# Optimization experiments

Hardware: AMD Instinct MI355X
Metric: run time of the kernel (lower is better)

The kernel has to match this reference:

```python
import jax, jax.numpy as jnp
import numpy as np

B, N, C = 8, 1025, 768
NUM_HEADS = 12
HEAD_DIM = C // NUM_HEADS  # 64, also depthwise-conv channel count
HW = (32, 32)              # N = 1 + 32*32 (cls token)
SCALE = HEAD_DIM ** -0.5
VALUE_MASK_FILL = -10000.0
LN_EPS = 1e-5


def setup_inputs() -> dict:
    key = jax.random.key(0)
    ks = jax.random.split(key, 12)
    s = 0.02
    inp = {
        "x": jax.random.normal(ks[0], (B, N, C), jnp.float32),
        "mask": jax.random.bernoulli(ks[1], 0.9, (B, N)),
        "Wq": jax.random.normal(ks[2], (C, C), jnp.float32) * s,
        "Wk": jax.random.normal(ks[3], (C, C), jnp.float32) * s,
        "Wv": jax.random.normal(ks[4], (C, C), jnp.float32) * s,
        "pool_q_w": jax.random.normal(ks[5], (HEAD_DIM, 1, 3, 3), jnp.float32) * s,
        "pool_k_w": jax.random.normal(ks[6], (HEAD_DIM, 1, 3, 3), jnp.float32) * s,
        "pool_v_w": jax.random.normal(ks[7], (HEAD_DIM, 1, 3, 3), jnp.float32) * s,
        "gq": jnp.ones((HEAD_DIM,), jnp.float32),
        "bq": jnp.zeros((HEAD_DIM,), jnp.float32),
        "gk": jnp.ones((HEAD_DIM,), jnp.float32),
        "bk": jnp.zeros((HEAD_DIM,), jnp.float32),
        "gv": jnp.ones((HEAD_DIM,), jnp.float32),
        "bv": jnp.zeros((HEAD_DIM,), jnp.float32),
        "Wp": jax.random.normal(ks[8], (C, C), jnp.float32) * s,
        "bp": jnp.zeros((C,), jnp.float32),
    }
    return inp


def _layernorm(t, g, b):
    m = jnp.mean(t, axis=-1, keepdims=True)
    v = jnp.var(t, axis=-1, keepdims=True)
    return (t - m) * jax.lax.rsqrt(v + LN_EPS) * g + b


def _depthwise(t, w):
    # t: [BH, D, H, W], w: [D, 1, 3, 3] depthwise, stride 1, SAME padding
    return jax.lax.conv_general_dilated(
        t, w, window_strides=(1, 1), padding="SAME",
        dimension_numbers=("NCHW", "OIHW", "NCHW"),
        feature_group_count=t.shape[1])


def _attn_pool(t, w, g, b):
    # t: [B, H, N, D] with leading cls token; pool spatial tokens, norm after
    Bb, Hh, Nn, D = t.shape
    cls_tok, spat = t[:, :, :1], t[:, :, 1:]
    Hs, Ws = HW
    spat = spat.reshape(Bb * Hh, Hs, Ws, D).transpose(0, 3, 1, 2)
    spat = _depthwise(spat, w)
    spat = spat.reshape(Bb, Hh, D, Hs * Ws).transpose(0, 1, 3, 2)
    t = jnp.concatenate([cls_tok, spat], axis=2)
    return _layernorm(t, g, b)


def reference(x, mask, Wq, Wk, Wv, pool_q_w, pool_k_w, pool_v_w,
              gq, bq, gk, bk, gv, bv, Wp, bp):
    Bb, Nn, Cc = x.shape
    # QKV projections (no bias), split heads -> [B, H, N, D]
    q = (x @ Wq.T).reshape(Bb, Nn, NUM_HEADS, HEAD_DIM).transpose(0, 2, 1, 3)
    k = (x @ Wk.T).reshape(Bb, Nn, NUM_HEADS, HEAD_DIM).transpose(0, 2, 1, 3)
    v = (x @ Wv.T).reshape(Bb, Nn, NUM_HEADS, HEAD_DIM).transpose(0, 2, 1, 3)
    q = _attn_pool(q, pool_q_w, gq, bq)
    k = _attn_pool(k, pool_k_w, gk, bk)
    v = _attn_pool(v, pool_v_w, gv, bv)
    attn = jnp.einsum("bhqd,bhkd->bhqk", q, k) * SCALE
    # mask: [B, N] bool; broadcast as (B,1,N,1), False -> value_mask_fill
    attn = jnp.where(mask[:, None, :, None], attn, VALUE_MASK_FILL)
    attn = jax.nn.softmax(attn, axis=-1)
    attn_origin = attn
    out = jnp.einsum("bhqk,bhkd->bhqd", attn, v)
    # residual pooling, skipping the cls token
    out = jnp.concatenate([out[:, :, :1], out[:, :, 1:] + q[:, :, 1:]], axis=2)
    out = out.transpose(0, 2, 1, 3).reshape(Bb, Nn, Cc)
    out = out @ Wp.T + bp
    return out, attn_origin
```

## Files before the change

### kernel.cpp

```cpp
#include <hip/hip_runtime.h>
#include <hip/hip_bf16.h>
#include <cstdint>
#include <cstddef>

typedef unsigned short u16;
typedef __attribute__((ext_vector_type(8))) short bf16x8;
typedef __attribute__((ext_vector_type(4))) float f32x4;

#define MFMA16(a,b,c) __builtin_amdgcn_mfma_f32_16x16x32_bf16(a,b,c,0,0,0)
#define GLL16(gp, lp) __builtin_amdgcn_global_load_lds( \
    (const __attribute__((address_space(1))) void*)(gp), \
    (__attribute__((address_space(3))) void*)(lp), 16, 0, 0)

static constexpr int kB = 8, kH = 12, kN = 1025, kC = 768, kD = 64;
static constexpr int kBH = kB*kH;
static constexpr int kNP = 1056;
static constexpr int kM  = kB*kN;
static constexpr float kScale = 0.125f;

__device__ __forceinline__ u16 f2b(float f){
  unsigned u = __builtin_bit_cast(unsigned, f);
  u = (u + 0x7fffu + ((u>>16)&1u)) >> 16;
  return (u16)u;
}
__device__ __forceinline__ float b2f(u16 s){
  unsigned u = ((unsigned)s)<<16;
  return __builtin_bit_cast(float, u);
}
__device__ __forceinline__ int xcd_swz(int orig, int nwg){
  int q = nwg>>3, r = nwg&7;
  int xcd = orig&7, idx = orig>>3;
  return (xcd<r ? xcd*(q+1) : r*(q+1)+(xcd-r)*q) + idx;
}

__global__ __launch_bounds__(256) void k_prep(const float4* __restrict__ x,
    const float* __restrict__ w0, const float* __restrict__ w1,
    const float* __restrict__ w2, const float* __restrict__ w3,
    const unsigned char* __restrict__ m,
    u16* __restrict__ xb, u16* __restrict__ wb, int* __restrict__ maskn){
  __shared__ int cnt;
  const int bid = blockIdx.x;
  if (bid < 6150){
    int i = bid*256 + threadIdx.x;
    float4 v = x[i];
    ushort4 o; o.x=f2b(v.x); o.y=f2b(v.y); o.z=f2b(v.z); o.w=f2b(v.w);
    *reinterpret_cast<ushort4*>(xb + (size_t)i*4) = o;
  } else if (bid < 8454){
    int j = (bid-6150)*256 + threadIdx.x;
    int sel = j/147456, i = j - sel*147456;
    const float* ws[4] = {w0,w1,w2,w3};
    float4 v = reinterpret_cast<const float4*>(ws[sel])[i];
    ushort4 o; o.x=f2b(v.x); o.y=f2b(v.y); o.z=f2b(v.z); o.w=f2b(v.w);
    *reinterpret_cast<ushort4*>(wb + (size_t)sel*589824 + (size_t)i*4) = o;
  } else {
    if (threadIdx.x==0) cnt = 0;
    __syncthreads();
    int local = 0;
    for (int i=threadIdx.x; i<1024; i+=256) local += (m[i]!=0);
    atomicAdd(&cnt, local);
    __syncthreads();
    bool b8 = (cnt > 512);
    int lb = bid - 8454;
    for (int i = lb*256 + threadIdx.x; i < kM; i += 32*256){
      int v = b8 ? (m[i]!=0) : (reinterpret_cast<const int*>(m)[i] != 0);
      maskn[i] = v;
    }
  }
}

template<int MODE>
__global__ __launch_bounds__(256) void k_gemm128(const u16* __restrict__ A,
      const u16* __restrict__ wb, const float* __restrict__ bias,
      u16* __restrict__ outb, float* __restrict__ outf){
  __shared__ union SM {
    struct { u16 a[128*32]; u16 b[128*32]; } s;
    u16 c2[64*136];
  } sm;
  constexpr int NB = (MODE==0) ? 18 : 6;
  const int wg = xcd_swz(blockIdx.x, gridDim.x);
  const int m0 = (wg / NB)*128;
  const int N0 = (wg % NB)*128;
  const int sel = (MODE==0) ? (N0/768) : 3;
  const int jb  = (MODE==0) ? (N0%768) : N0;
  const u16* W = wb + (size_t)sel*589824;
  const int t = threadIdx.x;
  const int wave = t>>6, lane = t&63;
  const int g = lane>>4, cl = lane&15;
  const int wr2 = (wave>>1)*64, wc2 = (wave&1)*64;

  const int cid0 = wave*64 + lane;
  const int cid1 = cid0 + 256;
  const int ar0 = m0 + (cid0>>2) < kM ? m0 + (cid0>>2) : kM-1;
  const int ar1 = m0 + (cid1>>2) < kM ? m0 + (cid1>>2) : kM-1;
  const int ac0 = (cid0&3)<<3, ac1 = (cid1&3)<<3;
  const int br0 = jb + (cid0>>2), br1 = jb + (cid1>>2);
  u16* lA0 = &sm.s.a[(wave*64)*8];
  u16* lA1 = &sm.s.a[(256 + wave*64)*8];
  u16* lB0 = &sm.s.b[(wave*64)*8];
  u16* lB1 = &sm.s.b[(256 + wave*64)*8];

  f32x4 acc[4][4];
  #pragma unroll
  for (int i=0;i<4;i++)
    #pragma unroll
    for (int j=0;j<4;j++) acc[i][j] = (f32x4){0.f,0.f,0.f,0.f};

  for (int k0=0; k0<768; k0+=32){
    __syncthreads();
    GLL16(A + (size_t)ar0*768 + k0 + ac0, lA0);
    GLL16(A + (size_t)ar1*768 + k0 + ac1, lA1);
    GLL16(W + (size_t)br0*768 + k0 + ac0, lB0);
    GLL16(W + (size_t)br1*768 + k0 + ac1, lB1);
    __syncthreads();
    bf16x8 af[4], bfg[4];
    #pragma unroll
    for (int fm=0; fm<4; fm++)
      af[fm] = *reinterpret_cast<const bf16x8*>(&sm.s.a[(wr2+fm*16+cl)*32 + g*8]);
    #pragma unroll
    for (int fn=0; fn<4; fn++)
      bfg[fn] = *reinterpret_cast<const bf16x8*>(&sm.s.b[(wc2+fn*16+cl)*32 + g*8]);
    #pragma unroll
    for (int fm=0; fm<4; fm++)
      #pragma unroll
      for (int fn=0; fn<4; fn++)
        acc[fm][fn] = MFMA16(af[fm], bfg[fn], acc[fm][fn]);
  }

  if (MODE==0){
    #pragma unroll
    for (int ph=0; ph<2; ++ph){
      __syncthreads();
      if ((wave>>1) == ph){
        #pragma unroll
        for (int fm=0; fm<4; fm++)
          #pragma unroll
          for (int fn=0; fn<4; fn++)
            #pragma unroll
            for (int i=0;i<4;i++){
              int r = fm*16 + g*4 + i;
              int c = wc2 + fn*16 + cl;
              sm.c2[r*136 + c] = f2b(acc[fm][fn][i]);
            }
      }
      __syncthreads();
      #pragma unroll
      for (int it=0; it<4; it++){
        int cid = t + it*256;
        int r = cid >> 4, cc = (cid & 15) * 8;
        int gm = m0 + ph*64 + r;
        if (gm < kM){
          *reinterpret_cast<uint4*>(&outb[(size_t)gm*2304 + N0 + cc]) =
              *reinterpret_cast<const uint4*>(&sm.c2[r*136 + cc]);
        }
      }
    }
  } else {
    #pragma unroll
    for (int fm=0; fm<4; fm++)
      #pragma unroll
      for (int fn=0; fn<4; fn++)
        #pragma unroll
        for (int i=0;i<4;i++){
          int gm = m0 + wr2 + fm*16 + g*4 + i;
          if (gm >= kM) continue;
          int gc = jb + wc2 + fn*16 + cl;
          outf[(size_t)gm*768 + gc] = acc[fm][fn][i] + bias[gc];
        }
  }
}

__global__ __launch_bounds__(256) void k_pool3(const u16* __restrict__ qkvmat,
    const float* __restrict__ wq, const float* __restrict__ wk, const float* __restrict__ wv,
    const float* __restrict__ gq, const float* __restrict__ bq,
    const float* __restrict__ gk, const float* __restrict__ bk,
    const float* __restrict__ gv, const float* __restrict__ bv,
    u16* __restrict__ Qp, u16* __restrict__ Kp, u16* __restrict__ Vt){
  __shared__ u16 vt[64][72];
  const int which = blockIdx.y;
  const float* w9 = (which==0)?wq:(which==1)?wk:wv;
  const float* gg = (which==0)?gq:(which==1)?gk:gv;
  const float* bb2= (which==0)?bq:(which==1)?bk:bv;
  u16* out = (which==0)?Qp:(which==1)?Kp:Vt;

  const int wave = threadIdx.x>>6, d = threadIdx.x&63;
  const int wg  = xcd_swz(blockIdx.x, 96*17);
  const int nb  = wg % 17;
  const int bh  = wg / 17;
  const int b = bh/12, h = bh - b*12;
  const int np0 = nb*64;
  const u16* base = qkvmat + ((size_t)b*1025)*2304 + which*768 + h*64;

  float wreg[9];
  #pragma unroll
  for (int j=0;j<9;j++) wreg[j] = w9[d*9+j];
  const float gd = gg[d], bd = bb2[d];

  for (int iter=0; iter<16; ++iter){
    const int np = np0 + iter*4 + wave;
    float v = 0.f;
    if (np < kN){
      if (np == 0){
        v = b2f(base[d]);
      } else {
        int y = (np-1)>>5, x = (np-1)&31;
        #pragma unroll
        for (int ky=0; ky<3; ky++){
          int yy = y+ky-1;
          if (yy<0 || yy>31) continue;
          #pragma unroll
          for (int kx=0; kx<3; kx++){
            int xx = x+kx-1;
            if (xx<0 || xx>31) continue;
            v += wreg[ky*3+kx] * b2f(base[(size_t)(1+yy*32+xx)*2304 + d]);
          }
        }
      }
      float s = v, s2 = v*v;
      #pragma unroll
      for (int off=1; off<64; off<<=1){ s += __shfl_xor(s, off); s2 += __shfl_xor(s2, off); }
      float mean = s*(1.f/64.f);
      float var  = s2*(1.f/64.f) - mean*mean;
      v = (v-mean)*rsqrtf(var+1e-5f)*gd + bd;
    }
    if (which==2) vt[d][iter*4+wave] = f2b(v);
    else if (np < kNP) out[((size_t)bh*kNP + np)*kD + d] = f2b(v);
  }

  if (which==2){
    __syncthreads();
    const int dr = threadIdx.x>>2, seg = threadIdx.x&3;
    if (np0 + seg*16 < kNP){
      u16* dst = Vt + ((size_t)bh*kD + dr)*kNP + np0 + seg*16;
      *reinterpret_cast<uint4*>(dst)     = *reinterpret_cast<const uint4*>(&vt[dr][seg*16]);
      *reinterpret_cast<uint4*>(dst + 8) = *reinterpret_cast<const uint4*>(&vt[dr][seg*16+8]);
    }
  }
}

__global__ __launch_bounds__(256) void k_attn(const u16* __restrict__ Qp, const u16* __restrict__ Kp,
    const u16* __restrict__ Vt, const int* __restrict__ maskn,
    float* __restrict__ attn_out, u16* __restrict__ ctx){
  constexpr int LDE = 1064;
  __shared__ u16 E[16*LDE];
  __shared__ float Lrow[16];
  __shared__ float Linv[16];
  const int wave = threadIdx.x>>6, lane = threadIdx.x&63;
  const int xcd  = blockIdx.x & 7;
  const int slot = blockIdx.x >> 3;
  const int bh = xcd*12 + slot/65;
  const int qt = slot%65;
  const int b  = bh / 12, h = bh - b*12;
  const int qbase = qt*16;
  const int g = lane>>4, cl = lane&15;

  if (threadIdx.x < 16) Lrow[threadIdx.x] = 0.f;
  __syncthreads();

  const u16* qrow = Qp + ((size_t)bh*kNP + (qbase + cl))*kD + g*8;
  bf16x8 aq0 = *reinterpret_cast<const bf16x8*>(qrow);
  bf16x8 aq1 = *reinterpret_cast<const bf16x8*>(qrow + 32);

  float mq[4];
  #pragma unroll
  for (int i=0;i<4;i++){
    int qi = qbase + g*4 + i;
    mq[i] = (qi<kN && maskn[b*kN+qi]!=0) ? kScale : 0.f;
  }

  const u16* kb = Kp + (size_t)bh*kNP*kD;
  float rsum[4] = {0.f,0.f,0.f,0.f};
  #pragma unroll 2
  for (int kt=wave; kt<33; kt+=4){
    const int ktb = kt*32;
    const u16* kr = kb + (size_t)(ktb+cl)*kD + g*8;
    bf16x8 b00 = *reinterpret_cast<const bf16x8*>(kr);
    bf16x8 b01 = *reinterpret_cast<const bf16x8*>(kr+32);
    bf16x8 b10 = *reinterpret_cast<const bf16x8*>(kr+1024);
    bf16x8 b11 = *reinterpret_cast<const bf16x8*>(kr+1024+32);
    f32x4 s0 = {0.f,0.f,0.f,0.f}, s1 = {0.f,0.f,0.f,0.f};
    __builtin_amdgcn_s_setprio(1);
    s0 = MFMA16(aq0,b00,s0); s0 = MFMA16(aq1,b01,s0);
    s1 = MFMA16(aq0,b10,s1); s1 = MFMA16(aq1,b11,s1);
    __builtin_amdgcn_s_setprio(0);
    const bool v0 = (ktb+cl)<kN, v1 = (ktb+16+cl)<kN;
    #pragma unroll
    for (int i=0;i<4;i++){
      int row = g*4+i;
      float e0 = v0 ? __expf(s0[i]*mq[i]) : 0.f;
      float e1 = v1 ? __expf(s1[i]*mq[i]) : 0.f;
      rsum[i] += e0 + e1;
      E[row*LDE + ktb + cl]      = f2b(e0);
      E[row*LDE + ktb + 16 + cl] = f2b(e1);
    }
  }
  #pragma unroll
  for (int off=1; off<16; off<<=1){
    #pragma unroll
    for (int i=0;i<4;i++) rsum[i] += __shfl_xor(rsum[i], off);
  }
  if (cl == 0){
    #pragma unroll
    for (int i=0;i<4;i++) atomicAdd(&Lrow[g*4+i], rsum[i]);
  }
  __syncthreads();
  if (threadIdx.x < 16) Linv[threadIdx.x] = 1.f/Lrow[threadIdx.x];
  __syncthreads();

  {
    size_t S = (size_t)bh*kN*kN + (size_t)qbase*kN;
    float* tp = attn_out + S;
    int rows = kN - qbase; if (rows > 16) rows = 16;
    int T = rows*kN;
    int head = (int)((4 - (S & 3)) & 3);
    int body4 = (T - head) >> 2;
    int tail = T - head - body4*4;
    int t = threadIdx.x;
    if (t < head){
      int e = t;
      unsigned row = ((unsigned)(e*16369))>>24;
      int col = e - (int)row*kN;
      tp[e] = b2f(E[row*LDE+col]) * Linv[row];
    }
    if (t < tail){
      int e = head + body4*4 + t;
      unsigned row = ((unsigned)(e*16369))>>24;
      int col = e - (int)row*kN;
      tp[e] = b2f(E[row*LDE+col]) * Linv[row];
    }
    for (int idx = t; idx < body4; idx += 256){
      int e = head + idx*4;
      unsigned row0 = ((unsigned)(e*16369))>>24;
      unsigned row3 = ((unsigned)((e+3)*16369))>>24;
      float4 vv;
      if (row0 == row3){
        int col = e - (int)row0*kN;
        const u16* ep = &E[row0*LDE + col];
        float li = Linv[row0];
        vv.x = b2f(ep[0])*li; vv.y = b2f(ep[1])*li;
        vv.z = b2f(ep[2])*li; vv.w = b2f(ep[3])*li;
      } else {
        float tmp[4];
        #pragma unroll
        for (int j=0;j<4;j++){
          int ee = e+j;
          unsigned row = ((unsigned)(ee*16369))>>24;
          int col = ee - (int)row*kN;
          tmp[j] = b2f(E[row*LDE+col]) * Linv[row];
        }
        vv.x=tmp[0]; vv.y=tmp[1]; vv.z=tmp[2]; vv.w=tmp[3];
      }
      *reinterpret_cast<float4*>(tp + e) = vv;
    }
  }

  const int d0 = wave*16;
  f32x4 oacc = (f32x4){0.f,0.f,0.f,0.f};
  const u16* vb = Vt + ((size_t)bh*kD + d0 + cl)*kNP;
  for (int kt0=0; kt0<32; kt0+=4){
    bf16x8 pa[4], vv[4];
    #pragma unroll
    for (int j=0;j<4;j++){
      const int ko = (kt0+j)*32 + g*8;
      pa[j] = *reinterpret_cast<const bf16x8*>(&E[cl*LDE + ko]);
      vv[j] = *reinterpret_cast<const bf16x8*>(vb + ko);
    }
    __builtin_amdgcn_s_setprio(1);
    #pragma unroll
    for (int j=0;j<4;j++) oacc = MFMA16(pa[j], vv[j], oacc);
    __builtin_amdgcn_s_setprio(0);
  }
  {
    const int ko = 32*32 + g*8;
    bf16x8 pa = *reinterpret_cast<const bf16x8*>(&E[cl*LDE + ko]);
    bf16x8 vv = *reinterpret_cast<const bf16x8*>(vb + ko);
    oacc = MFMA16(pa, vv, oacc);
  }
  #pragma unroll
  for (int i=0;i<4;i++){
    int row = g*4+i, qi = qbase+row;
    if (qi < kN){
      float val = oacc[i] * Linv[row];
      int dd = d0 + cl;
      if (qi >= 1) val += b2f(Qp[((size_t)bh*kNP + qi)*kD + dd]);
      ctx[((size_t)(b*kN + qi))*kC + h*kD + dd] = f2b(val);
    }
  }
}

extern "C" void kernel_launch(void* const* d_in, const int* in_sizes, int n_in,
                              void* d_out, int out_size, void* d_ws, size_t ws_size,
                              hipStream_t stream) {
  const float* x    = (const float*)d_in[0];
  const void*  msk  = d_in[1];
  const float* Wq   = (const float*)d_in[2];
  const float* Wk   = (const float*)d_in[3];
  const float* Wv   = (const float*)d_in[4];
  const float* pw_q = (const float*)d_in[5];
  const float* pw_k = (const float*)d_in[6];
  const float* pw_v = (const float*)d_in[7];
  const float* gq   = (const float*)d_in[8];
  const float* bq   = (const float*)d_in[9];
  const float* gk   = (const float*)d_in[10];
  const float* bk   = (const float*)d_in[11];
  const float* gv   = (const float*)d_in[12];
  const float* bv   = (const float*)d_in[13];
  const float* Wp   = (const float*)d_in[14];
  const float* bp   = (const float*)d_in[15];

  char* ws = (char*)d_ws;
  u16* xb     = (u16*)(ws + 0);
  u16* wb     = (u16*)(ws + 12595200);
  int* maskn  = (int*)(ws + 17313792);
  u16* qkvmat = (u16*)(ws + 17346816);
  u16* Qp     = (u16*)(ws + 55132416);
  u16* Kp     = (u16*)(ws + 68108544);
  u16* Vt     = (u16*)(ws + 81084672);
  u16* ctx    = (u16*)(ws + 17346816);

  float* out1 = (float*)d_out;
  float* attn = out1 + (size_t)kM*kC;

  k_prep<<<8486, 256, 0, stream>>>(reinterpret_cast<const float4*>(x),
                                   Wq, Wk, Wv, Wp, (const unsigned char*)msk,
                                   xb, wb, maskn);
  k_gemm128<0><<<65*18, 256, 0, stream>>>(xb, wb, nullptr, qkvmat, nullptr);
  k_pool3<<<dim3(96*17,3), 256, 0, stream>>>(qkvmat, pw_q, pw_k, pw_v,
                                             gq, bq, gk, bk, gv, bv, Qp, Kp, Vt);
  k_attn<<<96*65, 256, 0, stream>>>(Qp, Kp, Vt, maskn, attn, ctx);
  k_gemm128<1><<<65*6, 256, 0, stream>>>(ctx, wb, bp, nullptr, out1);
}
```

Measured before the change: 411.5 us.

## Transpose QK^T MFMA operands so each lane owns a query row

Swaps the MFMA A/B operands in the attention-score kernel so each lane holds four consecutive key scores for a single query row. Exponentials are then packed pairwise with v_cvt_pk_bf16_f32 and written to LDS as 8-byte vector stores instead of scalar u16 stores. The row-sum reduction drops from a 4-step shuffle on four accumulators to two shuffles on one value. The partial last key tile is peeled out and handled by wave 0, which removes per-element bounds checks from the main loop.

```diff
diff --git a/kernel.cpp b/kernel.cpp
--- a/kernel.cpp
+++ b/kernel.cpp
@@ -26,6 +26,11 @@
 __device__ __forceinline__ float b2f(u16 s){
   unsigned u = ((unsigned)s)<<16;
   return __builtin_bit_cast(float, u);
+}
+__device__ __forceinline__ unsigned pkbf(float a, float b){
+  unsigned r;
+  asm("v_cvt_pk_bf16_f32 %0, %1, %2" : "=v"(r) : "v"(a), "v"(b));
+  return r;
 }
 __device__ __forceinline__ int xcd_swz(int orig, int nwg){
   int q = nwg>>3, r = nwg&7;
@@ -260,17 +265,14 @@
   bf16x8 aq0 = *reinterpret_cast<const bf16x8*>(qrow);
   bf16x8 aq1 = *reinterpret_cast<const bf16x8*>(qrow + 32);
 
-  float mq[4];
-  #pragma unroll
-  for (int i=0;i<4;i++){
-    int qi = qbase + g*4 + i;
-    mq[i] = (qi<kN && maskn[b*kN+qi]!=0) ? kScale : 0.f;
-  }
+  const int qi_l = qbase + cl;
+  const float mqc = (qi_l < kN && maskn[b*kN + qi_l] != 0) ? kScale : 0.f;
 
   const u16* kb = Kp + (size_t)bh*kNP*kD;
-  float rsum[4] = {0.f,0.f,0.f,0.f};
+  float rsum = 0.f;
+  u16* erow = &E[cl*LDE];
   #pragma unroll 2
-  for (int kt=wave; kt<33; kt+=4){
+  for (int kt=wave; kt<32; kt+=4){
     const int ktb = kt*32;
     const u16* kr = kb + (size_t)(ktb+cl)*kD + g*8;
     bf16x8 b00 = *reinterpret_cast<const bf16x8*>(kr);
@@ -279,29 +281,36 @@
     bf16x8 b11 = *reinterpret_cast<const bf16x8*>(kr+1024+32);
     f32x4 s0 = {0.f,0.f,0.f,0.f}, s1 = {0.f,0.f,0.f,0.f};
     __builtin_amdgcn_s_setprio(1);
-    s0 = MFMA16(aq0,b00,s0); s0 = MFMA16(aq1,b01,s0);
-    s1 = MFMA16(aq0,b10,s1); s1 = MFMA16(aq1,b11,s1);
+    s0 = MFMA16(b00,aq0,s0); s0 = MFMA16(b01,aq1,s0);
+    s1 = MFMA16(b10,aq0,s1); s1 = MFMA16(b11,aq1,s1);
     __builtin_amdgcn_s_setprio(0);
-    const bool v0 = (ktb+cl)<kN, v1 = (ktb+16+cl)<kN;
-    #pragma unroll
-    for (int i=0;i<4;i++){
-      int row = g*4+i;
-      float e0 = v0 ? __expf(s0[i]*mq[i]) : 0.f;
-      float e1 = v1 ? __expf(s1[i]*mq[i]) : 0.f;
-      rsum[i] += e0 + e1;
-      E[row*LDE + ktb + cl]      = f2b(e0);
-      E[row*LDE + ktb + 16 + cl] = f2b(e1);
-    }
-  }
-  #pragma unroll
-  for (int off=1; off<16; off<<=1){
-    #pragma unroll
-    for (int i=0;i<4;i++) rsum[i] += __shfl_xor(rsum[i], off);
-  }
-  if (cl == 0){
-    #pragma unroll
-    for (int i=0;i<4;i++) atomicAdd(&Lrow[g*4+i], rsum[i]);
-  }
+    float e0 = __expf(s0[0]*mqc), e1 = __expf(s0[1]*mqc);
+    float e2 = __expf(s0[2]*mqc), e3 = __expf(s0[3]*mqc);
+    float f0 = __expf(s1[0]*mqc), f1 = __expf(s1[1]*mqc);
+    float f2 = __expf(s1[2]*mqc), f3 = __expf(s1[3]*mqc);
+    rsum += ((e0+e1)+(e2+e3)) + ((f0+f1)+(f2+f3));
+    uint2 w0v = { pkbf(e0,e1), pkbf(e2,e3) };
+    uint2 w1v = { pkbf(f0,f1), pkbf(f2,f3) };
+    *reinterpret_cast<uint2*>(&erow[ktb + 4*g])      = w0v;
+    *reinterpret_cast<uint2*>(&erow[ktb + 16 + 4*g]) = w1v;
+  }
+  if (wave == 0){
+    const int ktb = 1024;
+    const u16* kr = kb + (size_t)(ktb+cl)*kD + g*8;
+    bf16x8 b00 = *reinterpret_cast<const bf16x8*>(kr);
+    bf16x8 b01 = *reinterpret_cast<const bf16x8*>(kr+32);
+    f32x4 s0 = {0.f,0.f,0.f,0.f};
+    s0 = MFMA16(b00,aq0,s0); s0 = MFMA16(b01,aq1,s0);
+    float e0 = (g==0) ? __expf(s0[0]*mqc) : 0.f;
+    rsum += e0;
+    uint2 w0v = { pkbf(e0,0.f), 0u };
+    uint2 zz  = { 0u, 0u };
+    *reinterpret_cast<uint2*>(&erow[ktb + 4*g])      = w0v;
+    *reinterpret_cast<uint2*>(&erow[ktb + 16 + 4*g]) = zz;
+  }
+  rsum += __shfl_xor(rsum, 16);
+  rsum += __shfl_xor(rsum, 32);
+  if (lane < 16) atomicAdd(&Lrow[cl], rsum);
   __syncthreads();
   if (threadIdx.x < 16) Linv[threadIdx.x] = 1.f/Lrow[threadIdx.x];
   __syncthreads();
```

Result: no change. 406.8 us (-1.1%).
